# Kernel optimization log

Hardware: AMD Instinct MI355X
Metric: run time of the kernel (lower is better)

The kernel has to match this reference:

```python
import jax, jax.numpy as jnp
import numpy as np

NEG_SLOPE = 0.2

def leaky(x):
    return jnp.where(x >= 0, x, NEG_SLOPE * x)

def setup_inputs() -> dict:
    key = jax.random.key(0)
    ks = jax.random.split(key, 9)
    B, D, H = 2048, 128, 512
    s = lambda fan: 1.0 / np.sqrt(fan)
    return {
        "x":   jax.random.normal(ks[0], (B, D), jnp.float32),
        "We1": jax.random.normal(ks[1], (H, D), jnp.float32) * s(D),
        "be1": jax.random.normal(ks[2], (H,), jnp.float32) * s(D),
        "We2": jax.random.normal(ks[3], (D, H), jnp.float32) * s(H),
        "be2": jax.random.normal(ks[4], (D,), jnp.float32) * s(H),
        "W1s": jax.random.normal(ks[5], (D, H), jnp.float32),      # dec_j.linear1 weight (H,1) stacked -> (D,H)
        "b1s": jax.random.normal(ks[6], (D, H), jnp.float32) * 0.1,
        "W2s": jax.random.normal(ks[7], (D, D, H), jnp.float32) * s(H),  # dec_j.linear2 weight (D,H) stacked
        "b2s": jax.random.normal(ks[8], (D, D), jnp.float32) * s(H),
    }

def reference(x, We1, be1, We2, be2, W1s, b1s, W2s, b2s):
    # Encoder: D -> H -> D, tanh
    enc_h = leaky(x @ We1.T + be1)                     # (B,H)
    encoded = jnp.tanh(enc_h @ We2.T + be2)            # (B,D)
    # Per-feature decoders, vectorized over j: dec_j(encoded[:, j])
    z = encoded.T                                      # (D,B) latent scalar per decoder j
    hid = leaky(z[:, :, None] * W1s[:, None, :] + b1s[:, None, :])   # (D,B,H)
    terms = jnp.einsum('jbh,jdh->jbd', hid, W2s) + b2s[:, None, :]   # (D,B,D)
    # outputs[i] = sum_{j<=i} terms[j] -> inclusive prefix sum over j
    outputs = jnp.tanh(jnp.cumsum(terms, axis=0))      # (D,B,D)
    return outputs
```

## Files before the change

### kernel.cpp

```cpp
#include <hip/hip_runtime.h>

#define B_SZ 2048
#define D_SZ 128
#define H_SZ 512
#define JC 8
#define NCH 16
#define CPG 3
#define NGRP 5

typedef _Float16 half8 __attribute__((ext_vector_type(8)));
typedef float floatx4 __attribute__((ext_vector_type(4)));
typedef unsigned int uint4v __attribute__((ext_vector_type(4)));

static __device__ __forceinline__ float tanh_fast(float x) {
  float e = __expf(2.0f * x);
  return 1.0f - 2.0f * __builtin_amdgcn_rcpf(e + 1.0f);
}

static __device__ __forceinline__ void split_pair(float a, float b,
                                                  unsigned int& hi,
                                                  unsigned int& lo) {
  auto h = __builtin_amdgcn_cvt_pkrtz(a, b);
  float ra = a - (float)h[0];
  float rb = b - (float)h[1];
  auto l = __builtin_amdgcn_cvt_pkrtz(ra, rb);
  hi = __builtin_bit_cast(unsigned int, h);
  lo = __builtin_bit_cast(unsigned int, l);
}

__global__ __launch_bounds__(256) void prep_kernel(
    const float* __restrict__ W2s, _Float16* __restrict__ W2h,
    _Float16* __restrict__ W2l, const float* __restrict__ x,
    const float* __restrict__ We1, const float* __restrict__ be1,
    const float* __restrict__ We2, const float* __restrict__ be2,
    float* __restrict__ z) {
  const int t = threadIdx.x;
  if (blockIdx.x >= 256) {
    const int idx = (blockIdx.x - 256) * 256 + t;
    const int dl = idx & 63, kg = (idx >> 6) & 63, dtj = idx >> 12;
    const int d = (dtj & 1) * 64 + dl, j = dtj >> 1;
    const float* src = W2s + ((size_t)j * D_SZ + d) * H_SZ + kg * 8;
    float4 a = *(const float4*)src;
    float4 b = *(const float4*)(src + 4);
    unsigned int h0, l0, h1, l1, h2, l2, h3, l3;
    split_pair(a.x, a.y, h0, l0); split_pair(a.z, a.w, h1, l1);
    split_pair(b.x, b.y, h2, l2); split_pair(b.z, b.w, h3, l3);
    ((uint4*)W2h)[idx] = make_uint4(h0, h1, h2, h3);
    ((uint4*)W2l)[idx] = make_uint4(l0, l1, l2, l3);
    return;
  }
  __shared__ float xs[8][132];
  __shared__ float hs[8][516];
  const int b0 = blockIdx.x * 8;
  {
    int r = t >> 5, c4 = t & 31;
    float4 v = ((const float4*)(x + (size_t)(b0 + r) * D_SZ))[c4];
    xs[r][c4 * 4 + 0] = v.x; xs[r][c4 * 4 + 1] = v.y;
    xs[r][c4 * 4 + 2] = v.z; xs[r][c4 * 4 + 3] = v.w;
  }
  __syncthreads();
  for (int hb = 0; hb < 2; ++hb) {
    const int h = t + hb * 256;
    float acc[8];
    float bias = be1[h];
#pragma unroll
    for (int r = 0; r < 8; ++r) acc[r] = bias;
    const float4* wp = (const float4*)(We1 + (size_t)h * D_SZ);
    for (int k4 = 0; k4 < 32; ++k4) {
      float4 wv = wp[k4];
#pragma unroll
      for (int r = 0; r < 8; ++r) {
        acc[r] = fmaf(wv.x, xs[r][k4 * 4 + 0], acc[r]);
        acc[r] = fmaf(wv.y, xs[r][k4 * 4 + 1], acc[r]);
        acc[r] = fmaf(wv.z, xs[r][k4 * 4 + 2], acc[r]);
        acc[r] = fmaf(wv.w, xs[r][k4 * 4 + 3], acc[r]);
      }
    }
#pragma unroll
    for (int r = 0; r < 8; ++r) {
      float u = acc[r];
      hs[r][h] = fmaxf(u, 0.2f * u);
    }
  }
  __syncthreads();
  {
    const int d = t & 127, rg = t >> 7;
    float acc[4];
    float bias = be2[d];
#pragma unroll
    for (int r = 0; r < 4; ++r) acc[r] = bias;
    const float4* wp = (const float4*)(We2 + (size_t)d * H_SZ);
    for (int k4 = 0; k4 < 128; ++k4) {
      float4 wv = wp[k4];
#pragma unroll
      for (int r = 0; r < 4; ++r) {
        int row = rg * 4 + r;
        acc[r] = fmaf(wv.x, hs[row][k4 * 4 + 0], acc[r]);
        acc[r] = fmaf(wv.y, hs[row][k4 * 4 + 1], acc[r]);
        acc[r] = fmaf(wv.z, hs[row][k4 * 4 + 2], acc[r]);
        acc[r] = fmaf(wv.w, hs[row][k4 * 4 + 3], acc[r]);
      }
    }
#pragma unroll
    for (int r = 0; r < 4; ++r) {
      z[(size_t)d * B_SZ + b0 + rg * 4 + r] = tanh_fast(acc[r]);
    }
  }
}

__global__ __launch_bounds__(256, 2) void dec_kernel(
    const float* __restrict__ W1s, const float* __restrict__ b1s,
    const _Float16* __restrict__ W2h, const _Float16* __restrict__ W2l,
    const float* __restrict__ b2s, const float* __restrict__ z,
    float* __restrict__ out, float* __restrict__ T) {
  __shared__ float w1L[JC][512];
  __shared__ float b1L[JC][512];
  __shared__ float zL[JC][64];
  __shared__ float b2L[JC][128];

  const int t = threadIdx.x, bx = blockIdx.x;
  const int jc = bx & 15, bt = bx >> 4;
  const int b0 = bt * 64, j0 = jc * JC;

#pragma unroll
  for (int i = 0; i < 4; ++i) {
    int g = t + 256 * i;
    int jr = g >> 7, col = (g & 127) * 4;
    *(float4*)&w1L[jr][col] = *(const float4*)(W1s + (size_t)(j0 + jr) * H_SZ + col);
    *(float4*)&b1L[jr][col] = *(const float4*)(b1s + (size_t)(j0 + jr) * H_SZ + col);
  }
  if (t < 128) {
    int jr = t >> 4, col = (t & 15) * 4;
    *(float4*)&zL[jr][col] = *(const float4*)(z + (size_t)(j0 + jr) * B_SZ + b0 + col);
  }
  {
    int jr = t >> 5, col = (t & 31) * 4;
    *(float4*)&b2L[jr][col] = *(const float4*)(b2s + (size_t)(j0 + jr) * D_SZ + col);
  }
  __syncthreads();

  const int lane = t & 63;
  const int quad = lane >> 4, l16 = lane & 15;
  const int w = t >> 6;
  const int brow0 = w * 16 + l16;

  floatx4 acc[8][3];
#pragma unroll
  for (int d = 0; d < 8; ++d)
#pragma unroll
    for (int p = 0; p < 3; ++p) acc[d][p] = (floatx4){0.f, 0.f, 0.f, 0.f};
  float bc[8] = {0.f, 0.f, 0.f, 0.f, 0.f, 0.f, 0.f, 0.f};

  for (int jj = 0; jj < JC; ++jj) {
    const int j = j0 + jj;
    const unsigned int bb0 =
        (unsigned)(j * 2) * 32768u + (unsigned)(quad * 512 + l16 * 8);
    const float zv = zL[jj][brow0];

#pragma unroll 2
    for (int ks = 0; ks < 16; ++ks) {
      const int ko = ks * 32 + quad * 8;
      float4 wa = *(const float4*)&w1L[jj][ko];
      float4 wc = *(const float4*)&w1L[jj][ko + 4];
      float4 ba = *(const float4*)&b1L[jj][ko];
      float4 bb = *(const float4*)&b1L[jj][ko + 4];
      const unsigned int off0 = bb0 + (unsigned)(ks * 2048);
      const unsigned int off1 = off0 + 32768u;
      half8 fh0 = *(const half8*)(W2h + off0);
      half8 fh1 = *(const half8*)(W2h + off0 + 128);
      half8 fh2 = *(const half8*)(W2h + off0 + 256);
      half8 fh3 = *(const half8*)(W2h + off0 + 384);
      half8 gh0 = *(const half8*)(W2h + off1);
      half8 gh1 = *(const half8*)(W2h + off1 + 128);
      half8 gh2 = *(const half8*)(W2h + off1 + 256);
      half8 gh3 = *(const half8*)(W2h + off1 + 384);
      half8 fl0 = *(const half8*)(W2l + off0);
      half8 fl1 = *(const half8*)(W2l + off0 + 128);
      half8 fl2 = *(const half8*)(W2l + off0 + 256);
      half8 fl3 = *(const half8*)(W2l + off0 + 384);
      half8 gl0 = *(const half8*)(W2l + off1);
      half8 gl1 = *(const half8*)(W2l + off1 + 128);
      half8 gl2 = *(const half8*)(W2l + off1 + 256);
      half8 gl3 = *(const half8*)(W2l + off1 + 384);

      float h0 = fmaf(zv, wa.x, ba.x), h1 = fmaf(zv, wa.y, ba.y);
      float h2 = fmaf(zv, wa.z, ba.z), h3 = fmaf(zv, wa.w, ba.w);
      float h4 = fmaf(zv, wc.x, bb.x), h5 = fmaf(zv, wc.y, bb.y);
      float h6 = fmaf(zv, wc.z, bb.z), h7 = fmaf(zv, wc.w, bb.w);
      h0 = fmaxf(h0, 0.2f * h0); h1 = fmaxf(h1, 0.2f * h1);
      h2 = fmaxf(h2, 0.2f * h2); h3 = fmaxf(h3, 0.2f * h3);
      h4 = fmaxf(h4, 0.2f * h4); h5 = fmaxf(h5, 0.2f * h5);
      h6 = fmaxf(h6, 0.2f * h6); h7 = fmaxf(h7, 0.2f * h7);
      unsigned int a0, a1, a2, a3, x0, x1, x2, x3;
      split_pair(h0, h1, a0, x0); split_pair(h2, h3, a1, x1);
      split_pair(h4, h5, a2, x2); split_pair(h6, h7, a3, x3);
      half8 fah = __builtin_bit_cast(half8, (uint4v){a0, a1, a2, a3});
      half8 fal = __builtin_bit_cast(half8, (uint4v){x0, x1, x2, x3});

      acc[0][0] = __builtin_amdgcn_mfma_f32_16x16x32_f16(fah, fh0, acc[0][0], 0, 0, 0);
      acc[0][1] = __builtin_amdgcn_mfma_f32_16x16x32_f16(fah, fl0, acc[0][1], 0, 0, 0);
      acc[0][2] = __builtin_amdgcn_mfma_f32_16x16x32_f16(fal, fh0, acc[0][2], 0, 0, 0);
      acc[1][0] = __builtin_amdgcn_mfma_f32_16x16x32_f16(fah, fh1, acc[1][0], 0, 0, 0);
      acc[1][1] = __builtin_amdgcn_mfma_f32_16x16x32_f16(fah, fl1, acc[1][1], 0, 0, 0);
      acc[1][2] = __builtin_amdgcn_mfma_f32_16x16x32_f16(fal, fh1, acc[1][2], 0, 0, 0);
      acc[2][0] = __builtin_amdgcn_mfma_f32_16x16x32_f16(fah, fh2, acc[2][0], 0, 0, 0);
      acc[2][1] = __builtin_amdgcn_mfma_f32_16x16x32_f16(fah, fl2, acc[2][1], 0, 0, 0);
      acc[2][2] = __builtin_amdgcn_mfma_f32_16x16x32_f16(fal, fh2, acc[2][2], 0, 0, 0);
      acc[3][0] = __builtin_amdgcn_mfma_f32_16x16x32_f16(fah, fh3, acc[3][0], 0, 0, 0);
      acc[3][1] = __builtin_amdgcn_mfma_f32_16x16x32_f16(fah, fl3, acc[3][1], 0, 0, 0);
      acc[3][2] = __builtin_amdgcn_mfma_f32_16x16x32_f16(fal, fh3, acc[3][2], 0, 0, 0);
      acc[4][0] = __builtin_amdgcn_mfma_f32_16x16x32_f16(fah, gh0, acc[4][0], 0, 0, 0);
      acc[4][1] = __builtin_amdgcn_mfma_f32_16x16x32_f16(fah, gl0, acc[4][1], 0, 0, 0);
      acc[4][2] = __builtin_amdgcn_mfma_f32_16x16x32_f16(fal, gh0, acc[4][2], 0, 0, 0);
      acc[5][0] = __builtin_amdgcn_mfma_f32_16x16x32_f16(fah, gh1, acc[5][0], 0, 0, 0);
      acc[5][1] = __builtin_amdgcn_mfma_f32_16x16x32_f16(fah, gl1, acc[5][1], 0, 0, 0);
      acc[5][2] = __builtin_amdgcn_mfma_f32_16x16x32_f16(fal, gh1, acc[5][2], 0, 0, 0);
      acc[6][0] = __builtin_amdgcn_mfma_f32_16x16x32_f16(fah, gh2, acc[6][0], 0, 0, 0);
      acc[6][1] = __builtin_amdgcn_mfma_f32_16x16x32_f16(fah, gl2, acc[6][1], 0, 0, 0);
      acc[6][2] = __builtin_amdgcn_mfma_f32_16x16x32_f16(fal, gh2, acc[6][2], 0, 0, 0);
      acc[7][0] = __builtin_amdgcn_mfma_f32_16x16x32_f16(fah, gh3, acc[7][0], 0, 0, 0);
      acc[7][1] = __builtin_amdgcn_mfma_f32_16x16x32_f16(fah, gl3, acc[7][1], 0, 0, 0);
      acc[7][2] = __builtin_amdgcn_mfma_f32_16x16x32_f16(fal, gh3, acc[7][2], 0, 0, 0);
    }

#pragma unroll
    for (int df = 0; df < 8; ++df) bc[df] += b2L[jj][df * 16 + l16];

    float* obase = out + (size_t)j * (B_SZ * D_SZ) + l16;
    const int brow = b0 + w * 16 + quad * 4;
    float* orow0 = obase + (size_t)brow * D_SZ;
#pragma unroll
    for (int r = 0; r < 4; ++r) {
#pragma unroll
      for (int df = 0; df < 8; ++df) {
        float s = (acc[df][0][r] + acc[df][1][r]) + (acc[df][2][r] + bc[df]);
        if (jc == 0) s = tanh_fast(s);
        orow0[(size_t)r * D_SZ + df * 16] = s;
      }
    }
  }

  if (jc < NCH - 1) {
    float* tbase = T + (size_t)jc * (B_SZ * D_SZ) + l16;
    const int brow = b0 + w * 16 + quad * 4;
    float* trow0 = tbase + (size_t)brow * D_SZ;
#pragma unroll
    for (int r = 0; r < 4; ++r) {
#pragma unroll
      for (int df = 0; df < 8; ++df) {
        trow0[(size_t)r * D_SZ + df * 16] =
            (acc[df][0][r] + acc[df][1][r]) + (acc[df][2][r] + bc[df]);
      }
    }
  }
}

__global__ __launch_bounds__(256) void fixup_kernel(
    const float* __restrict__ T, float* __restrict__ out) {
  const int idx = blockIdx.x * 256 + threadIdx.x;
  const int d4 = idx & 31;
  const int b = (idx >> 5) & (B_SZ - 1);
  const int q = idx >> 16;
  const size_t stride = B_SZ * (D_SZ / 4);
  const size_t tix = (size_t)b * (D_SZ / 4) + d4;
  const float4* T4 = (const float4*)T;
  float4* O4 = (float4*)out;

  const int c0 = 1 + q * CPG;
  float4 carry = make_float4(0.f, 0.f, 0.f, 0.f);
  for (int c = 0; c < c0; ++c) {
    float4 tv = T4[(size_t)c * stride + tix];
    carry.x += tv.x; carry.y += tv.y; carry.z += tv.z; carry.w += tv.w;
  }
#pragma unroll
  for (int cc = 0; cc < CPG; ++cc) {
    const int c = c0 + cc;
    if (cc > 0) {
      float4 tv = T4[(size_t)(c - 1) * stride + tix];
      carry.x += tv.x; carry.y += tv.y; carry.z += tv.z; carry.w += tv.w;
    }
#pragma unroll
    for (int jj = 0; jj < JC; ++jj) {
      const int j = c * JC + jj;
      const size_t oix = ((size_t)j * B_SZ + b) * (D_SZ / 4) + d4;
      float4 s = O4[oix];
      s.x = tanh_fast(s.x + carry.x);
      s.y = tanh_fast(s.y + carry.y);
      s.z = tanh_fast(s.z + carry.z);
      s.w = tanh_fast(s.w + carry.w);
      O4[oix] = s;
    }
  }
}

extern "C" void kernel_launch(void* const* d_in, const int* in_sizes, int n_in,
                              void* d_out, int out_size, void* d_ws,
                              size_t ws_size, hipStream_t stream) {
  (void)in_sizes; (void)n_in; (void)out_size; (void)ws_size;
  const float* x   = (const float*)d_in[0];
  const float* We1 = (const float*)d_in[1];
  const float* be1 = (const float*)d_in[2];
  const float* We2 = (const float*)d_in[3];
  const float* be2 = (const float*)d_in[4];
  const float* W1s = (const float*)d_in[5];
  const float* b1s = (const float*)d_in[6];
  const float* W2s = (const float*)d_in[7];
  const float* b2s = (const float*)d_in[8];
  float* out = (float*)d_out;

  float* zws = (float*)d_ws;
  _Float16* W2h = (_Float16*)((char*)d_ws + (1u << 20));
  _Float16* W2l = (_Float16*)((char*)d_ws + (1u << 20) + (1u << 24));
  float* T = (float*)((char*)d_ws + (1u << 20) + (2u << 24));

  prep_kernel<<<4352, 256, 0, stream>>>(W2s, W2h, W2l, x, We1, be1, We2, be2, zws);
  dec_kernel<<<512, 256, 0, stream>>>(W1s, b1s, W2h, W2l, b2s, zws, out, T);
  fixup_kernel<<<NGRP * 256, 256, 0, stream>>>(T, out);
}
```

Baseline: 368.7 us.

## Split W2 columns across wave pairs and share A fragments via LDS

Each wave now loads only half of the W2 output columns (64 of 128) and computes those columns for two 16-row batch tiles: its own, plus its partner wave's, whose split fp16 hidden activations arrive through double-buffered LDS. This halves the per-wave global W2 fragment traffic and register footprint for B operands. In exchange it adds an LDS write/read and a block-wide __syncthreads every k-step, which may stall the MFMA pipeline.

```diff
diff --git a/kernel.cpp b/kernel.cpp
--- a/kernel.cpp
+++ b/kernel.cpp
@@ -117,6 +117,8 @@
   __shared__ float b1L[JC][512];
   __shared__ float zL[JC][64];
   __shared__ float b2L[JC][128];
+  __shared__ uint4v aHs[2][4][64];
+  __shared__ uint4v aLs[2][4][64];
 
   const int t = threadIdx.x, bx = blockIdx.x;
   const int jc = bx & 15, bt = bx >> 4;
@@ -142,46 +144,42 @@
   const int lane = t & 63;
   const int quad = lane >> 4, l16 = lane & 15;
   const int w = t >> 6;
-  const int brow0 = w * 16 + l16;
-
-  floatx4 acc[8][3];
-#pragma unroll
-  for (int d = 0; d < 8; ++d)
-#pragma unroll
-    for (int p = 0; p < 3; ++p) acc[d][p] = (floatx4){0.f, 0.f, 0.f, 0.f};
-  float bc[8] = {0.f, 0.f, 0.f, 0.f, 0.f, 0.f, 0.f, 0.f};
+  const int h = w & 1;
+  const int pw = w ^ 1;
+
+  floatx4 acc[2][4][3];
+#pragma unroll
+  for (int a = 0; a < 2; ++a)
+#pragma unroll
+    for (int b = 0; b < 4; ++b)
+#pragma unroll
+      for (int p = 0; p < 3; ++p) acc[a][b][p] = (floatx4){0.f, 0.f, 0.f, 0.f};
+  float bc[4] = {0.f, 0.f, 0.f, 0.f};
 
   for (int jj = 0; jj < JC; ++jj) {
     const int j = j0 + jj;
     const unsigned int bb0 =
-        (unsigned)(j * 2) * 32768u + (unsigned)(quad * 512 + l16 * 8);
-    const float zv = zL[jj][brow0];
+        (unsigned)(j * 2 + h) * 32768u + (unsigned)(quad * 512 + l16 * 8);
+    const float zv = zL[jj][w * 16 + l16];
 
 #pragma unroll 2
     for (int ks = 0; ks < 16; ++ks) {
+      const int par = ks & 1;
+      const unsigned int off = bb0 + (unsigned)(ks * 2048);
+      half8 fh0 = *(const half8*)(W2h + off);
+      half8 fh1 = *(const half8*)(W2h + off + 128);
+      half8 fh2 = *(const half8*)(W2h + off + 256);
+      half8 fh3 = *(const half8*)(W2h + off + 384);
+      half8 fl0 = *(const half8*)(W2l + off);
+      half8 fl1 = *(const half8*)(W2l + off + 128);
+      half8 fl2 = *(const half8*)(W2l + off + 256);
+      half8 fl3 = *(const half8*)(W2l + off + 384);
+
       const int ko = ks * 32 + quad * 8;
       float4 wa = *(const float4*)&w1L[jj][ko];
       float4 wc = *(const float4*)&w1L[jj][ko + 4];
       float4 ba = *(const float4*)&b1L[jj][ko];
       float4 bb = *(const float4*)&b1L[jj][ko + 4];
-      const unsigned int off0 = bb0 + (unsigned)(ks * 2048);
-      const unsigned int off1 = off0 + 32768u;
-      half8 fh0 = *(const half8*)(W2h + off0);
-      half8 fh1 = *(const half8*)(W2h + off0 + 128);
-      half8 fh2 = *(const half8*)(W2h + off0 + 256);
-      half8 fh3 = *(const half8*)(W2h + off0 + 384);
-      half8 gh0 = *(const half8*)(W2h + off1);
-      half8 gh1 = *(const half8*)(W2h + off1 + 128);
-      half8 gh2 = *(const half8*)(W2h + off1 + 256);
-      half8 gh3 = *(const half8*)(W2h + off1 + 384);
-      half8 fl0 = *(const half8*)(W2l + off0);
-      half8 fl1 = *(const half8*)(W2l + off0 + 128);
-      half8 fl2 = *(const half8*)(W2l + off0 + 256);
-      half8 fl3 = *(const half8*)(W2l + off0 + 384);
-      half8 gl0 = *(const half8*)(W2l + off1);
-      half8 gl1 = *(const half8*)(W2l + off1 + 128);
-      half8 gl2 = *(const half8*)(W2l + off1 + 256);
-      half8 gl3 = *(const half8*)(W2l + off1 + 384);
 
       float h0 = fmaf(zv, wa.x, ba.x), h1 = fmaf(zv, wa.y, ba.y);
       float h2 = fmaf(zv, wa.z, ba.z), h3 = fmaf(zv, wa.w, ba.w);
@@ -197,59 +195,77 @@
       half8 fah = __builtin_bit_cast(half8, (uint4v){a0, a1, a2, a3});
       half8 fal = __builtin_bit_cast(half8, (uint4v){x0, x1, x2, x3});
 
-      acc[0][0] = __builtin_amdgcn_mfma_f32_16x16x32_f16(fah, fh0, acc[0][0], 0, 0, 0);
-      acc[0][1] = __builtin_amdgcn_mfma_f32_16x16x32_f16(fah, fl0, acc[0][1], 0, 0, 0);
-      acc[0][2] = __builtin_amdgcn_mfma_f32_16x16x32_f16(fal, fh0, acc[0][2], 0, 0, 0);
-      acc[1][0] = __builtin_amdgcn_mfma_f32_16x16x32_f16(fah, fh1, acc[1][0], 0, 0, 0);
-      acc[1][1] = __builtin_amdgcn_mfma_f32_16x16x32_f16(fah, fl1, acc[1][1], 0, 0, 0);
-      acc[1][2] = __builtin_amdgcn_mfma_f32_16x16x32_f16(fal, fh1, acc[1][2], 0, 0, 0);
-      acc[2][0] = __builtin_amdgcn_mfma_f32_16x16x32_f16(fah, fh2, acc[2][0], 0, 0, 0);
-      acc[2][1] = __builtin_amdgcn_mfma_f32_16x16x32_f16(fah, fl2, acc[2][1], 0, 0, 0);
-      acc[2][2] = __builtin_amdgcn_mfma_f32_16x16x32_f16(fal, fh2, acc[2][2], 0, 0, 0);
-      acc[3][0] = __builtin_amdgcn_mfma_f32_16x16x32_f16(fah, fh3, acc[3][0], 0, 0, 0);
-      acc[3][1] = __builtin_amdgcn_mfma_f32_16x16x32_f16(fah, fl3, acc[3][1], 0, 0, 0);
-      acc[3][2] = __builtin_amdgcn_mfma_f32_16x16x32_f16(fal, fh3, acc[3][2], 0, 0, 0);
-      acc[4][0] = __builtin_amdgcn_mfma_f32_16x16x32_f16(fah, gh0, acc[4][0], 0, 0, 0);
-      acc[4][1] = __builtin_amdgcn_mfma_f32_16x16x32_f16(fah, gl0, acc[4][1], 0, 0, 0);
-      acc[4][2] = __builtin_amdgcn_mfma_f32_16x16x32_f16(fal, gh0, acc[4][2], 0, 0, 0);
-      acc[5][0] = __builtin_amdgcn_mfma_f32_16x16x32_f16(fah, gh1, acc[5][0], 0, 0, 0);
-      acc[5][1] = __builtin_amdgcn_mfma_f32_16x16x32_f16(fah, gl1, acc[5][1], 0, 0, 0);
-      acc[5][2] = __builtin_amdgcn_mfma_f32_16x16x32_f16(fal, gh1, acc[5][2], 0, 0, 0);
-      acc[6][0] = __builtin_amdgcn_mfma_f32_16x16x32_f16(fah, gh2, acc[6][0], 0, 0, 0);
-      acc[6][1] = __builtin_amdgcn_mfma_f32_16x16x32_f16(fah, gl2, acc[6][1], 0, 0, 0);
-      acc[6][2] = __builtin_amdgcn_mfma_f32_16x16x32_f16(fal, gh2, acc[6][2], 0, 0, 0);
-      acc[7][0] = __builtin_amdgcn_mfma_f32_16x16x32_f16(fah, gh3, acc[7][0], 0, 0, 0);
-      acc[7][1] = __builtin_amdgcn_mfma_f32_16x16x32_f16(fah, gl3, acc[7][1], 0, 0, 0);
-      acc[7][2] = __builtin_amdgcn_mfma_f32_16x16x32_f16(fal, gh3, acc[7][2], 0, 0, 0);
-    }
-
-#pragma unroll
-    for (int df = 0; df < 8; ++df) bc[df] += b2L[jj][df * 16 + l16];
-
-    float* obase = out + (size_t)j * (B_SZ * D_SZ) + l16;
-    const int brow = b0 + w * 16 + quad * 4;
-    float* orow0 = obase + (size_t)brow * D_SZ;
-#pragma unroll
-    for (int r = 0; r < 4; ++r) {
-#pragma unroll
-      for (int df = 0; df < 8; ++df) {
-        float s = (acc[df][0][r] + acc[df][1][r]) + (acc[df][2][r] + bc[df]);
-        if (jc == 0) s = tanh_fast(s);
-        orow0[(size_t)r * D_SZ + df * 16] = s;
+      aHs[par][w][lane] = (uint4v){a0, a1, a2, a3};
+      aLs[par][w][lane] = (uint4v){x0, x1, x2, x3};
+      __syncthreads();
+      half8 pah = __builtin_bit_cast(half8, aHs[par][pw][lane]);
+      half8 pal = __builtin_bit_cast(half8, aLs[par][pw][lane]);
+
+      acc[0][0][0] = __builtin_amdgcn_mfma_f32_16x16x32_f16(fah, fh0, acc[0][0][0], 0, 0, 0);
+      acc[0][0][1] = __builtin_amdgcn_mfma_f32_16x16x32_f16(fah, fl0, acc[0][0][1], 0, 0, 0);
+      acc[0][0][2] = __builtin_amdgcn_mfma_f32_16x16x32_f16(fal, fh0, acc[0][0][2], 0, 0, 0);
+      acc[0][1][0] = __builtin_amdgcn_mfma_f32_16x16x32_f16(fah, fh1, acc[0][1][0], 0, 0, 0);
+      acc[0][1][1] = __builtin_amdgcn_mfma_f32_16x16x32_f16(fah, fl1, acc[0][1][1], 0, 0, 0);
+      acc[0][1][2] = __builtin_amdgcn_mfma_f32_16x16x32_f16(fal, fh1, acc[0][1][2], 0, 0, 0);
+      acc[0][2][0] = __builtin_amdgcn_mfma_f32_16x16x32_f16(fah, fh2, acc[0][2][0], 0, 0, 0);
+      acc[0][2][1] = __builtin_amdgcn_mfma_f32_16x16x32_f16(fah, fl2, acc[0][2][1], 0, 0, 0);
+      acc[0][2][2] = __builtin_amdgcn_mfma_f32_16x16x32_f16(fal, fh2, acc[0][2][2], 0, 0, 0);
+      acc[0][3][0] = __builtin_amdgcn_mfma_f32_16x16x32_f16(fah, fh3, acc[0][3][0], 0, 0, 0);
+      acc[0][3][1] = __builtin_amdgcn_mfma_f32_16x16x32_f16(fah, fl3, acc[0][3][1], 0, 0, 0);
+      acc[0][3][2] = __builtin_amdgcn_mfma_f32_16x16x32_f16(fal, fh3, acc[0][3][2], 0, 0, 0);
+      acc[1][0][0] = __builtin_amdgcn_mfma_f32_16x16x32_f16(pah, fh0, acc[1][0][0], 0, 0, 0);
+      acc[1][0][1] = __builtin_amdgcn_mfma_f32_16x16x32_f16(pah, fl0, acc[1][0][1], 0, 0, 0);
+      acc[1][0][2] = __builtin_amdgcn_mfma_f32_16x16x32_f16(pal, fh0, acc[1][0][2], 0, 0, 0);
+      acc[1][1][0] = __builtin_amdgcn_mfma_f32_16x16x32_f16(pah, fh1, acc[1][1][0], 0, 0, 0);
+      acc[1][1][1] = __builtin_amdgcn_mfma_f32_16x16x32_f16(pah, fl1, acc[1][1][1], 0, 0, 0);
+      acc[1][1][2] = __builtin_amdgcn_mfma_f32_16x16x32_f16(pal, fh1, acc[1][1][2], 0, 0, 0);
+      acc[1][2][0] = __builtin_amdgcn_mfma_f32_16x16x32_f16(pah, fh2, acc[1][2][0], 0, 0, 0);
+      acc[1][2][1] = __builtin_amdgcn_mfma_f32_16x16x32_f16(pah, fl2, acc[1][2][1], 0, 0, 0);
+      acc[1][2][2] = __builtin_amdgcn_mfma_f32_16x16x32_f16(pal, fh2, acc[1][2][2], 0, 0, 0);
+      acc[1][3][0] = __builtin_amdgcn_mfma_f32_16x16x32_f16(pah, fh3, acc[1][3][0], 0, 0, 0);
+      acc[1][3][1] = __builtin_amdgcn_mfma_f32_16x16x32_f16(pah, fl3, acc[1][3][1], 0, 0, 0);
+      acc[1][3][2] = __builtin_amdgcn_mfma_f32_16x16x32_f16(pal, fh3, acc[1][3][2], 0, 0, 0);
+    }
+
+#pragma unroll
+    for (int df = 0; df < 4; ++df) bc[df] += b2L[jj][h * 64 + df * 16 + l16];
+
+    const int dcol = h * 64 + l16;
+    float* obase = out + (size_t)j * (B_SZ * D_SZ) + dcol;
+#pragma unroll
+    for (int bf = 0; bf < 2; ++bf) {
+      const int rb = bf ? pw : w;
+      const int brow = b0 + rb * 16 + quad * 4;
+      float* orow = obase + (size_t)brow * D_SZ;
+#pragma unroll
+      for (int r = 0; r < 4; ++r) {
+#pragma unroll
+        for (int df = 0; df < 4; ++df) {
+          float s = (acc[bf][df][0][r] + acc[bf][df][1][r]) +
+                    (acc[bf][df][2][r] + bc[df]);
+          if (jc == 0) s = tanh_fast(s);
+          orow[(size_t)r * D_SZ + df * 16] = s;
+        }
       }
     }
   }
 
   if (jc < NCH - 1) {
-    float* tbase = T + (size_t)jc * (B_SZ * D_SZ) + l16;
-    const int brow = b0 + w * 16 + quad * 4;
-    float* trow0 = tbase + (size_t)brow * D_SZ;
-#pragma unroll
-    for (int r = 0; r < 4; ++r) {
-#pragma unroll
-      for (int df = 0; df < 8; ++df) {
-        trow0[(size_t)r * D_SZ + df * 16] =
-            (acc[df][0][r] + acc[df][1][r]) + (acc[df][2][r] + bc[df]);
+    const int dcol = h * 64 + l16;
+    float* tbase = T + (size_t)jc * (B_SZ * D_SZ) + dcol;
+#pragma unroll
+    for (int bf = 0; bf < 2; ++bf) {
+      const int rb = bf ? pw : w;
+      const int brow = b0 + rb * 16 + quad * 4;
+      float* trow = tbase + (size_t)brow * D_SZ;
+#pragma unroll
+      for (int r = 0; r < 4; ++r) {
+#pragma unroll
+        for (int df = 0; df < 4; ++df) {
+          trow[(size_t)r * D_SZ + df * 16] =
+              (acc[bf][df][0][r] + acc[bf][df][1][r]) +
+              (acc[bf][df][2][r] + bc[df]);
+        }
       }
     }
   }
```

New measurement: 340.8 us. 7.6% less time.
